# Performance work log

Hardware: AMD Instinct MI355X
Metric: run time of the kernel (lower is better)

Reference implementation:

```python
import jax, jax.numpy as jnp
import numpy as np

H = 32
W = 32
CIN = 64
GR = 4
CC = 6  # channels_count
N = 2


def build_a(h, w):
    # Faithful replication of the torch buffer construction (incl. overlapping
    # writes into channel 0, which accumulate multiple -1 entries per row).
    num = h * w
    a = np.zeros((num, CC, num), np.float32)
    for i in range(num):
        if (i + 1) % w != 0 and i + 1 < num:
            a[i, 0, i] = 1.0
            a[i, 0, i + 1] = -1.0
        if i + w < num:
            a[i, 1, i] = 1.0
            a[i, 1, i + w] = -1.0
        if (i + 2) % w != 0 and (i + 1) % w != 0 and (i + 2 < num):
            a[i, 2, i] = 1.0
            a[i, 2, i + 2] = -1.0
        if i + 2 * w < num:
            a[i, 3, i] = 1.0
            a[i, 3, i + 2 * w] = -1.0
        if i % w != 0 and i + w < num:
            a[i, 0, i] = 1.0
            a[i, 0, i + w - 1] = -1.0
        if (i + 1) % w != 0 and i + w < num:
            a[i, 0, i] = 1.0
            a[i, 0, i + w + 1] = -1.0
    for k in range(CC):
        a[-1, k, -1] = 1.0
    return jnp.asarray(a)


def conv2d(x, w, b, pad):
    y = jax.lax.conv_general_dilated(
        x, w, window_strides=(1, 1), padding=[(pad, pad), (pad, pad)],
        dimension_numbers=('NCHW', 'OIHW', 'NCHW'))
    return y + b[None, :, None, None]


def setup_inputs() -> dict:
    key = jax.random.key(0)
    ks = jax.random.split(key, 20)
    s = 0.05
    d = {
        'x': jax.random.normal(ks[0], (N, CIN, H, W), jnp.float32),
        'a': build_a(H, W),
        # grad branch: conv3x3 CIN->CIN, conv3x3 CIN->CC*GR
        'gw1': jax.random.normal(ks[1], (CIN, CIN, 3, 3), jnp.float32) * s,
        'gb1': jnp.zeros((CIN,), jnp.float32),
        'gw2': jax.random.normal(ks[2], (CC * GR, CIN, 3, 3), jnp.float32) * s,
        'gb2': jnp.zeros((CC * GR,), jnp.float32),
        # att branch (sigmoid at end)
        'aw1': jax.random.normal(ks[3], (CIN, CIN, 3, 3), jnp.float32) * s,
        'ab1': jnp.zeros((CIN,), jnp.float32),
        'aw2': jax.random.normal(ks[4], (CC * GR, CIN, 3, 3), jnp.float32) * s,
        'ab2': jnp.zeros((CC * GR,), jnp.float32),
        # SE branch: 1x1 CIN->CIN//2, 1x1 CIN//2->GR
        'sw1': jax.random.normal(ks[5], (CIN // 2, CIN, 1, 1), jnp.float32) * s,
        'sb1': jnp.zeros((CIN // 2,), jnp.float32),
        'sw2': jax.random.normal(ks[6], (GR, CIN // 2, 1, 1), jnp.float32) * s,
        'sb2': jnp.zeros((GR,), jnp.float32),
        # GroupNorm(1, GR) affine params
        'gn_g': jnp.ones((GR,), jnp.float32),
        'gn_b': jnp.zeros((GR,), jnp.float32),
        # post conv3x3 GR->128
        'pw': jax.random.normal(ks[7], (128, GR, 3, 3), jnp.float32) * s,
        'pb': jnp.zeros((128,), jnp.float32),
    }
    return d


def reference(x, a, gw1, gb1, gw2, gb2, aw1, ab1, aw2, ab2,
              sw1, sb1, sw2, sb2, gn_g, gn_b, pw, pb):
    n, c, h, w = x.shape
    hw = h * w
    lrelu = lambda t: jax.nn.leaky_relu(t, 0.01)

    att = jax.nn.sigmoid(conv2d(lrelu(conv2d(x, aw1, ab1, 1)), aw2, ab2, 1))
    grad = conv2d(lrelu(conv2d(x, gw1, gb1, 1)), gw2, gb2, 1)
    pooled = jnp.mean(x, axis=(2, 3), keepdims=True)
    se = jax.nn.sigmoid(conv2d(lrelu(conv2d(pooled, sw1, sb1, 0)), sw2, sb2, 0))  # [n,GR,1,1]

    b = n * GR
    att = att.reshape(b, CC, hw, 1).transpose(0, 2, 1, 3)   # [b, hw, CC, 1]
    grad = grad.reshape(b, CC, hw, 1).transpose(0, 2, 1, 3)  # [b, hw, CC, 1]

    A = (a[None] * att).reshape(b, hw * CC, hw)   # [b, hw*CC, hw]
    B = (grad * att).reshape(b, hw * CC)          # [b, hw*CC]

    ATA = jnp.einsum('bkm,bkn->bmn', A, A) + 1e-12 * jnp.eye(hw, dtype=x.dtype)
    ATB = jnp.einsum('bkm,bk->bm', A, B)[..., None]
    sol = jnp.linalg.solve(ATA, ATB).reshape(n, GR, h, w)

    # GroupNorm(1, GR): normalize over all (GR,h,w) per sample, per-channel affine
    mu = jnp.mean(sol, axis=(1, 2, 3), keepdims=True)
    var = jnp.var(sol, axis=(1, 2, 3), keepdims=True)
    y = (sol - mu) / jnp.sqrt(var + 1e-5)
    y = y * gn_g[None, :, None, None] + gn_b[None, :, None, None]

    y = se * y
    return conv2d(y, pw, pb, 1)
```

## Files before the change

kernel.cpp:

```cpp
#include <hip/hip_runtime.h>
#include <math.h>

#define HW 1024

__device__ __forceinline__ float lrelu(float v) { return v > 0.f ? v : 0.01f * v; }
__device__ __forceinline__ float sigmoidf(float v) { return 1.f / (1.f + expf(-v)); }

__device__ __forceinline__ float block_reduce(float v, float* red, int tid) {
#pragma unroll
  for (int off = 32; off > 0; off >>= 1) v += __shfl_xor(v, off, 64);
  if ((tid & 63) == 0) red[tid >> 6] = v;
  __syncthreads();
  float s = red[0] + red[1] + red[2] + red[3];
  __syncthreads();
  return s;
}

template <int MODE>
__device__ __forceinline__ void conv_direct(
    const float* __restrict__ X,
    const float* __restrict__ Wb,
    float bias,
    float* __restrict__ outp,
    int rb) {
  __shared__ float4 sred[192];
  int tid = threadIdx.x;
  int w = tid >> 6, l = tid & 63;
  int c4 = l & 7, ry = l >> 3;
  int r = rb * 8 + ry;
  int c0 = c4 * 4;
  int cL = (c4 == 0) ? 0 : c0 - 1;
  int cR = (c4 == 7) ? 31 : c0 + 4;
  float lmf = (c4 == 0) ? 0.f : 1.f;
  float rmf = (c4 == 7) ? 0.f : 1.f;
  int rrc[3];
  float rmk[3];
#pragma unroll
  for (int dr = 0; dr < 3; ++dr) {
    int rr = r - 1 + dr;
    bool ok = (unsigned)rr < 32u;
    rrc[dr] = ok ? rr * 32 : 0;
    rmk[dr] = ok ? 1.f : 0.f;
  }
  const float* Xw = X + w * 16 * HW;
  const float* Wp = Wb + w * 16 * 9;
  float ax = 0.f, ay = 0.f, az = 0.f, aq = 0.f;
#pragma unroll 4
  for (int i = 0; i < 16; ++i) {
    const float* pl = Xw + i * HW;
    const float* wq = Wp + i * 9;
#pragma unroll
    for (int dr = 0; dr < 3; ++dr) {
      const float* rp = pl + rrc[dr];
      float4 m = *(const float4*)(rp + c0);
      float L = rp[cL] * lmf;
      float R = rp[cR] * rmf;
      float w0 = wq[dr * 3 + 0] * rmk[dr];
      float w1 = wq[dr * 3 + 1] * rmk[dr];
      float w2 = wq[dr * 3 + 2] * rmk[dr];
      ax += w0 * L   + w1 * m.x + w2 * m.y;
      ay += w0 * m.x + w1 * m.y + w2 * m.z;
      az += w0 * m.y + w1 * m.z + w2 * m.w;
      aq += w0 * m.z + w1 * m.w + w2 * R;
    }
  }
  if (w > 0) sred[(w - 1) * 64 + l] = make_float4(ax, ay, az, aq);
  __syncthreads();
  if (w == 0) {
    float4 p0 = sred[l], p1 = sred[64 + l], p2 = sred[128 + l];
    float o0 = ax + p0.x + p1.x + p2.x + bias;
    float o1 = ay + p0.y + p1.y + p2.y + bias;
    float o2 = az + p0.z + p1.z + p2.z + bias;
    float o3 = aq + p0.w + p1.w + p2.w + bias;
    if (MODE == 0) { o0 = lrelu(o0); o1 = lrelu(o1); o2 = lrelu(o2); o3 = lrelu(o3); }
    else if (MODE == 1) { o0 = sigmoidf(o0); o1 = sigmoidf(o1); o2 = sigmoidf(o2); o3 = sigmoidf(o3); }
    *(float4*)(outp + r * 32 + c0) = make_float4(o0, o1, o2, o3);
  }
}

__global__ __launch_bounds__(256) void conv64_pool(const float* __restrict__ x,
    const float* __restrict__ aw, const float* __restrict__ ab,
    const float* __restrict__ gw, const float* __restrict__ gb,
    float* __restrict__ t1, float* __restrict__ pooled) {
  int bx = blockIdx.x;
  if (bx < 1024) {
    int co = bx & 63, t = bx >> 6, rb = t & 3, g = t >> 2;
    int br = g >> 1, n = g & 1;
    conv_direct<0>(x + n * 64 * HW,
                   (br ? gw : aw) + co * 576,
                   (br ? gb : ab)[co],
                   t1 + (g * 64 + co) * HW, rb);
  } else {
    __shared__ float red[4];
    int p = bx - 1024;
    const float* px = x + p * HW;
    int tid = threadIdx.x;
    float s = px[tid] + px[tid + 256] + px[tid + 512] + px[tid + 768];
    s = block_reduce(s, red, tid);
    if (tid == 0) pooled[p] = s * (1.f / 1024.f);
  }
}

__global__ __launch_bounds__(256) void conv24_k(const float* __restrict__ t1,
    const float* __restrict__ aw2, const float* __restrict__ ab2,
    const float* __restrict__ gw2, const float* __restrict__ gb2,
    float* __restrict__ attb, float* __restrict__ gradb) {
  int bx = blockIdx.x;
  int co = bx % 24, t = bx / 24, rb = t & 3, g = t >> 2;
  int br = g >> 1, n = g & 1;
  const float* X = t1 + g * 64 * HW;
  const float* Wb = (br ? gw2 : aw2) + co * 576;
  float bias = (br ? gb2 : ab2)[co];
  float* outp = (br ? gradb : attb) + (n * 24 + co) * HW;
  if (br) conv_direct<2>(X, Wb, bias, outp, rb);
  else    conv_direct<1>(X, Wb, bias, outp, rb);
}

__global__ __launch_bounds__(256, 1) void cg_solve(const float* __restrict__ att,
    const float* __restrict__ grad, float* __restrict__ sol,
    int maxit, float tolrel) {
  int b = blockIdx.x, tid = threadIdx.x;
  __shared__ float As[7 * 1088];
  __shared__ __align__(16) float ubuf[1152];
  __shared__ float red[8];
  float* OD1  = As;
  float* OD2  = As + 1 * 1088;
  float* OD30 = As + 2 * 1088;
  float* OD31 = As + 3 * 1088;
  float* OD32 = As + 4 * 1088;
  float* OD33 = As + 5 * 1088;
  float* OD64 = As + 6 * 1088;
  for (int i = tid; i < 448; i += 256) As[(i >> 6) * 1088 + (i & 63)] = 0.f;
  if (tid < 64) { ubuf[tid] = 0.f; ubuf[1088 + tid] = 0.f; }

  const float* attb = att + b * 6 * HW;
  const float* grdb = grad + b * 6 * HW;
  const int m0 = 4 * tid;
  const int idx0 = 64 + m0;
  float rk[4], d0v[4];
#pragma unroll
  for (int k = 0; k < 4; ++k) {
    int m = m0 + k;
    int mr = m & 31;
    bool p1 = (mr != 31) && (m < 1023);
    bool p2 = (mr != 0) && (m < 992);
    bool p3 = (mr != 31) && (m < 992);
    bool dd = p1 | p2 | p3;
    bool c1 = m < 992;
    bool c2 = (mr != 30) && (mr != 31) && (m < 1022);
    bool c3 = m < 960;
    float a0 = attb[m],            g0 = grdb[m];
    float a1 = attb[HW + m],       g1 = grdb[HW + m];
    float a2 = attb[2 * HW + m],   g2 = grdb[2 * HW + m];
    float a3 = attb[3 * HW + m],   g3 = grdb[3 * HW + m];
    float u0 = a0 * a0, t0 = u0 * g0;
    float u1 = a1 * a1, t1 = u1 * g1;
    float u2 = a2 * a2, t2 = u2 * g2;
    float u3 = a3 * a3, t3 = u3 * g3;
    float u0m1 = 0.f, t0m1 = 0.f; bool p1m1 = false, p2m1 = false, p3m1 = false;
    if (m >= 1) {
      int j = m - 1; int jr = j & 31;
      p1m1 = (jr != 31) && (j < 1023); p2m1 = (jr != 0) && (j < 992); p3m1 = (jr != 31) && (j < 992);
      float a = attb[j], g = grdb[j]; u0m1 = a * a; t0m1 = u0m1 * g;
    }
    float u0m31 = 0.f, t0m31 = 0.f; bool p2m31 = false, p3m31 = false;
    if (m >= 31) {
      int j = m - 31; int jr = j & 31;
      p2m31 = (jr != 0) && (j < 992); p3m31 = (jr != 31) && (j < 992);
      float a = attb[j], g = grdb[j]; u0m31 = a * a; t0m31 = u0m31 * g;
    }
    float u0m33 = 0.f, t0m33 = 0.f; bool p3m33 = false;
    if (m >= 33) {
      int j = m - 33; int jr = j & 31;
      p3m33 = (jr != 31) && (j < 992);
      float a = attb[j], g = grdb[j]; u0m33 = a * a; t0m33 = u0m33 * g;
    }
    float u1m32 = 0.f, t1m32 = 0.f; bool c1m32 = false;
    if (m >= 32) {
      int j = m - 32; c1m32 = (j < 992);
      float a = attb[HW + j], g = grdb[HW + j]; u1m32 = a * a; t1m32 = u1m32 * g;
    }
    float u2m2 = 0.f, t2m2 = 0.f; bool c2m2 = false;
    if (m >= 2) {
      int j = m - 2; int jr = j & 31;
      c2m2 = (jr != 30) && (jr != 31) && (j < 1022);
      float a = attb[2 * HW + j], g = grdb[2 * HW + j]; u2m2 = a * a; t2m2 = u2m2 * g;
    }
    float u3m64 = 0.f, t3m64 = 0.f; bool c3m64 = false;
    if (m >= 64) {
      int j = m - 64; c3m64 = (j < 960);
      float a = attb[3 * HW + j], g = grdb[3 * HW + j]; u3m64 = a * a; t3m64 = u3m64 * g;
    }
    float d0 = (dd ? u0 : 0.f) + (c1 ? u1 : 0.f) + (c2 ? u2 : 0.f) + (c3 ? u3 : 0.f)
             + (p1m1 ? u0m1 : 0.f) + (p2m31 ? u0m31 : 0.f) + (p3m33 ? u0m33 : 0.f)
             + (c1m32 ? u1m32 : 0.f) + (c2m2 ? u2m2 : 0.f) + (c3m64 ? u3m64 : 0.f) + 1e-12f;
    float rhs = (dd ? t0 : 0.f) + (c1 ? t1 : 0.f) + (c2 ? t2 : 0.f) + (c3 ? t3 : 0.f)
              - (p1m1 ? t0m1 : 0.f) - (p2m31 ? t0m31 : 0.f) - (p3m33 ? t0m33 : 0.f)
              - (c1m32 ? t1m32 : 0.f) - (c2m2 ? t2m2 : 0.f) - (c3m64 ? t3m64 : 0.f);
    if (m == 1023) {
      float a4 = attb[4 * HW + 1023], g4 = grdb[4 * HW + 1023];
      float a5 = attb[5 * HW + 1023], g5 = grdb[5 * HW + 1023];
      d0 += u0 + u1 + u2 + u3 + a4 * a4 + a5 * a5;
      rhs += t0 + t1 + t2 + t3 + a4 * a4 * g4 + a5 * a5 * g5;
    }
    int idx = idx0 + k;
    OD1[idx]  = p1 ? -u0 : 0.f;
    OD31[idx] = p2 ? -u0 : 0.f;
    OD33[idx] = p3 ? -u0 : 0.f;
    OD2[idx]  = (c2 ? -u2 : 0.f) + ((p2m31 && p3m31) ? u0m31 : 0.f);
    OD30[idx] = (p1m1 && p2m1) ? u0m1 : 0.f;
    OD32[idx] = (c1 ? -u1 : 0.f) + ((p1m1 && p3m1) ? u0m1 : 0.f);
    OD64[idx] = c3 ? -u3 : 0.f;
    d0v[k] = d0;
    rk[k] = rhs;
  }
  __syncthreads();

  float c1p[4], c1m[4], c2p[4], c2m[4], c30p[4], c30m[4], c31p[4], c31m[4];
  float c32p[4], c32m[4], c33p[4], c33m[4], c64p[4], c64m[4];
#pragma unroll
  for (int k = 0; k < 4; ++k) {
    int idx = idx0 + k;
    c1p[k]  = OD1[idx];  c1m[k]  = OD1[idx - 1];
    c2p[k]  = OD2[idx];  c2m[k]  = OD2[idx - 2];
    c30p[k] = OD30[idx]; c30m[k] = OD30[idx - 30];
    c31p[k] = OD31[idx]; c31m[k] = OD31[idx - 31];
    c32p[k] = OD32[idx]; c32m[k] = OD32[idx - 32];
    c33p[k] = OD33[idx]; c33m[k] = OD33[idx - 33];
    c64p[k] = OD64[idx]; c64m[k] = OD64[idx - 64];
  }

  float xk[4] = {0.f, 0.f, 0.f, 0.f};
  float uk[4], wk[4], pk[4], sk[4];
  const float* base = ubuf + idx0;
  int wv = tid >> 6, lane = tid & 63;

#define SPMV_AND_DOTS(GAM, DLT)                                              \
  {                                                                          \
    float2 A01 = *(const float2*)(base - 2);                                 \
    float2 A67 = *(const float2*)(base + 4);                                 \
    float2 B01 = *(const float2*)(base + 30);                                \
    float4 B25 = *(const float4*)(base + 32);                                \
    float  B6  = base[36];                                                   \
    float  C0  = base[-33];                                                  \
    float4 C14 = *(const float4*)(base - 32);                                \
    float2 C56 = *(const float2*)(base - 28);                                \
    float4 Dp  = *(const float4*)(base + 64);                                \
    float4 Ep  = *(const float4*)(base - 64);                                \
    float Aa[8] = {A01.x, A01.y, uk[0], uk[1], uk[2], uk[3], A67.x, A67.y};  \
    float Ba[7] = {B01.x, B01.y, B25.x, B25.y, B25.z, B25.w, B6};            \
    float Ca[7] = {C0, C14.x, C14.y, C14.z, C14.w, C56.x, C56.y};            \
    float Da[4] = {Dp.x, Dp.y, Dp.z, Dp.w};                                  \
    float Ea[4] = {Ep.x, Ep.y, Ep.z, Ep.w};                                  \
    GAM = 0.f; DLT = 0.f;                                                    \
    _Pragma("unroll")                                                        \
    for (int k = 0; k < 4; ++k) {                                            \
      float v = d0v[k] * uk[k];                                              \
      v += c1p[k]  * Aa[3 + k] + c1m[k]  * Aa[1 + k];                        \
      v += c2p[k]  * Aa[4 + k] + c2m[k]  * Aa[k];                            \
      v += c30p[k] * Ba[k]     + c30m[k] * Ca[3 + k];                        \
      v += c31p[k] * Ba[1 + k] + c31m[k] * Ca[2 + k];                        \
      v += c32p[k] * Ba[2 + k] + c32m[k] * Ca[1 + k];                        \
      v += c33p[k] * Ba[3 + k] + c33m[k] * Ca[k];                            \
      v += c64p[k] * Da[k]     + c64m[k] * Ea[k];                            \
      wk[k] = v;                                                             \
      GAM += rk[k] * uk[k];                                                  \
      DLT += v * uk[k];                                                      \
    }                                                                        \
    _Pragma("unroll")                                                        \
    for (int off = 32; off > 0; off >>= 1) {                                 \
      GAM += __shfl_xor(GAM, off, 64);                                       \
      DLT += __shfl_xor(DLT, off, 64);                                       \
    }                                                                        \
    if (lane == 0) { red[wv] = GAM; red[4 + wv] = DLT; }                     \
    __syncthreads();                                                         \
    GAM = red[0] + red[1] + red[2] + red[3];                                 \
    DLT = red[4] + red[5] + red[6] + red[7];                                 \
  }

#pragma unroll
  for (int k = 0; k < 4; ++k) uk[k] = rk[k] / d0v[k];
  *(float4*)(ubuf + idx0) = make_float4(uk[0], uk[1], uk[2], uk[3]);
  __syncthreads();
  float gamma, delta;
  SPMV_AND_DOTS(gamma, delta);
  if (!(fabsf(delta) > 0.f)) { goto done; }
  {
    float alpha = gamma / delta;
    float stop = gamma * tolrel;
#pragma unroll
    for (int k = 0; k < 4; ++k) {
      pk[k] = uk[k]; sk[k] = wk[k];
      xk[k] += alpha * pk[k];
      rk[k] -= alpha * sk[k];
    }
    float gamma_prev = gamma, alpha_prev = alpha;
    for (int it = 1; it < maxit; ++it) {
#pragma unroll
      for (int k = 0; k < 4; ++k) uk[k] = rk[k] / d0v[k];
      *(float4*)(ubuf + idx0) = make_float4(uk[0], uk[1], uk[2], uk[3]);
      __syncthreads();
      float g, dlt;
      SPMV_AND_DOTS(g, dlt);
      float beta = g / gamma_prev;
      float denom = dlt - beta * g / alpha_prev;
      if (!(fabsf(denom) > 0.f)) break;
      float alpha = g / denom;
#pragma unroll
      for (int k = 0; k < 4; ++k) {
        pk[k] = uk[k] + beta * pk[k];
        sk[k] = wk[k] + beta * sk[k];
        xk[k] += alpha * pk[k];
        rk[k] -= alpha * sk[k];
      }
      gamma_prev = g; alpha_prev = alpha;
      if (!(g > stop)) break;
    }
  }
done:
#pragma unroll
  for (int k = 0; k < 4; ++k) sol[b * HW + m0 + k] = xk[k];
#undef SPMV_AND_DOTS
}

__global__ __launch_bounds__(256) void gnorm_postconv(
    const float* __restrict__ sol, const float* __restrict__ pooled,
    const float* __restrict__ sw1, const float* __restrict__ sb1,
    const float* __restrict__ sw2, const float* __restrict__ sb2,
    const float* __restrict__ gn_g, const float* __restrict__ gn_b,
    const float* __restrict__ pw, const float* __restrict__ pb,
    float* __restrict__ out) {
  int bx = blockIdx.x;
  int n = bx >> 7, co = bx & 127;
  int tid = threadIdx.x;
  __shared__ float yp[4 * 1024];
  __shared__ float wb[36];
  __shared__ float red[4];
  __shared__ float s1[32];
  __shared__ float seg[4];
  if (tid < 36) wb[tid] = pw[co * 36 + tid];
  const float* s = sol + n * 4096;
  float v[16];
  float sum = 0.f, ssq = 0.f;
#pragma unroll
  for (int k = 0; k < 16; ++k) {
    v[k] = s[tid + 256 * k];
    sum += v[k];
    ssq += v[k] * v[k];
  }
  sum = block_reduce(sum, red, tid);
  ssq = block_reduce(ssq, red, tid);
  if (tid < 32) {
    float acc = sb1[tid];
    for (int ci = 0; ci < 64; ++ci) acc += sw1[tid * 64 + ci] * pooled[n * 64 + ci];
    s1[tid] = lrelu(acc);
  }
  __syncthreads();
  if (tid < 4) {
    float acc = sb2[tid];
    for (int j = 0; j < 32; ++j) acc += sw2[tid * 32 + j] * s1[j];
    seg[tid] = sigmoidf(acc);
  }
  __syncthreads();
  float mu = sum * (1.f / 4096.f);
  float var = ssq * (1.f / 4096.f) - mu * mu;
  float inv = rsqrtf(var + 1e-5f);
#pragma unroll
  for (int k = 0; k < 16; ++k) {
    int m = tid + 256 * k;
    int g = m >> 10;
    float val = (v[k] - mu) * inv * gn_g[g] + gn_b[g];
    yp[m] = val * seg[g];
  }
  __syncthreads();
  float bias = pb[co];
  float acc[4] = {bias, bias, bias, bias};
#pragma unroll
  for (int k = 0; k < 4; ++k) {
    int m = tid + 256 * k;
    int yy = m >> 5, xx = m & 31;
#pragma unroll
    for (int g = 0; g < 4; ++g) {
      const float* pl = yp + g * 1024;
      const float* wc = wb + g * 9;
#pragma unroll
      for (int dy = -1; dy <= 1; ++dy) {
        int y2 = yy + dy;
        if ((unsigned)y2 < 32u) {
          const float* row = pl + y2 * 32;
#pragma unroll
          for (int dx = -1; dx <= 1; ++dx) {
            int x2 = xx + dx;
            if ((unsigned)x2 < 32u) acc[k] += row[x2] * wc[(dy + 1) * 3 + dx + 1];
          }
        }
      }
    }
  }
#pragma unroll
  for (int k = 0; k < 4; ++k) out[(n * 128 + co) * HW + tid + 256 * k] = acc[k];
}

extern "C" void kernel_launch(void* const* d_in, const int* in_sizes, int n_in,
                              void* d_out, int out_size, void* d_ws, size_t ws_size,
                              hipStream_t stream) {
  const float* x   = (const float*)d_in[0];
  const float* gw1 = (const float*)d_in[2];
  const float* gb1 = (const float*)d_in[3];
  const float* gw2 = (const float*)d_in[4];
  const float* gb2 = (const float*)d_in[5];
  const float* aw1 = (const float*)d_in[6];
  const float* ab1 = (const float*)d_in[7];
  const float* aw2 = (const float*)d_in[8];
  const float* ab2 = (const float*)d_in[9];
  const float* sw1 = (const float*)d_in[10];
  const float* sb1 = (const float*)d_in[11];
  const float* sw2 = (const float*)d_in[12];
  const float* sb2 = (const float*)d_in[13];
  const float* gng = (const float*)d_in[14];
  const float* gnb = (const float*)d_in[15];
  const float* pw  = (const float*)d_in[16];
  const float* pb  = (const float*)d_in[17];
  float* out = (float*)d_out;
  float* ws = (float*)d_ws;

  float* t1     = out;
  float* attb   = ws;
  float* gradb  = ws + 49152;
  float* pooled = ws + 98304;
  float* solv   = ws + 98432;

  conv64_pool<<<1152, 256, 0, stream>>>(x, aw1, ab1, gw1, gb1, t1, pooled);
  conv24_k<<<384, 256, 0, stream>>>(t1, aw2, ab2, gw2, gb2, attb, gradb);
  cg_solve<<<8, 256, 0, stream>>>(attb, gradb, solv, 2000, 1e-5f);
  gnorm_postconv<<<256, 256, 0, stream>>>(solv, pooled, sw1, sb1, sw2, sb2,
                                          gng, gnb, pw, pb, out);
}
```

Baseline: 185.8 us.

## Cap CG iterations, stage conv weights in LDS, use DPP neighbor exchange

Lowers the CG iteration cap from 2000 to 600, which cuts worst-case solver work if convergence needs more iterations. The conv kernel now stages weights in shared memory and gets its left and right halo values from neighbouring lanes through DPP row shifts instead of extra global loads. The CG solver precomputes reciprocal diagonals and multiplies instead of dividing. The groupnorm kernel uses float4 loads with a fused scale and shift. The iteration cap can stop the solve before it meets tolerance, and the added syncs in the conv kernel bring a small cost of their own.

After: 150.9 us (median of 2 runs). -18.8%, faster.

```diff
diff --git a/kernel.cpp b/kernel.cpp
--- a/kernel.cpp
+++ b/kernel.cpp
@@ -5,6 +5,15 @@
 
 __device__ __forceinline__ float lrelu(float v) { return v > 0.f ? v : 0.01f * v; }
 __device__ __forceinline__ float sigmoidf(float v) { return 1.f / (1.f + expf(-v)); }
+
+__device__ __forceinline__ float dpp_prev(float x) {
+  return __int_as_float(__builtin_amdgcn_update_dpp(
+      0, __float_as_int(x), 0x111, 0xF, 0xF, true));
+}
+__device__ __forceinline__ float dpp_next(float x) {
+  return __int_as_float(__builtin_amdgcn_update_dpp(
+      0, __float_as_int(x), 0x101, 0xF, 0xF, true));
+}
 
 __device__ __forceinline__ float block_reduce(float v, float* red, int tid) {
 #pragma unroll
@@ -24,15 +33,15 @@
     float* __restrict__ outp,
     int rb) {
   __shared__ float4 sred[192];
+  __shared__ float wl[576];
   int tid = threadIdx.x;
   int w = tid >> 6, l = tid & 63;
   int c4 = l & 7, ry = l >> 3;
   int r = rb * 8 + ry;
   int c0 = c4 * 4;
-  int cL = (c4 == 0) ? 0 : c0 - 1;
-  int cR = (c4 == 7) ? 31 : c0 + 4;
   float lmf = (c4 == 0) ? 0.f : 1.f;
   float rmf = (c4 == 7) ? 0.f : 1.f;
+  if (tid < 144) ((float4*)wl)[tid] = ((const float4*)Wb)[tid];
   int rrc[3];
   float rmk[3];
 #pragma unroll
@@ -42,8 +51,9 @@
     rrc[dr] = ok ? rr * 32 : 0;
     rmk[dr] = ok ? 1.f : 0.f;
   }
+  __syncthreads();
   const float* Xw = X + w * 16 * HW;
-  const float* Wp = Wb + w * 16 * 9;
+  const float* Wp = wl + w * 144;
   float ax = 0.f, ay = 0.f, az = 0.f, aq = 0.f;
 #pragma unroll 4
   for (int i = 0; i < 16; ++i) {
@@ -53,8 +63,8 @@
     for (int dr = 0; dr < 3; ++dr) {
       const float* rp = pl + rrc[dr];
       float4 m = *(const float4*)(rp + c0);
-      float L = rp[cL] * lmf;
-      float R = rp[cR] * rmf;
+      float L = dpp_prev(m.w) * lmf;
+      float R = dpp_next(m.x) * rmf;
       float w0 = wq[dr * 3 + 0] * rmk[dr];
       float w1 = wq[dr * 3 + 1] * rmk[dr];
       float w2 = wq[dr * 3 + 2] * rmk[dr];
@@ -64,6 +74,7 @@
       aq += w0 * m.z + w1 * m.w + w2 * R;
     }
   }
+  __syncthreads();
   if (w > 0) sred[(w - 1) * 64 + l] = make_float4(ax, ay, az, aq);
   __syncthreads();
   if (w == 0) {
@@ -137,7 +148,7 @@
   const float* grdb = grad + b * 6 * HW;
   const int m0 = 4 * tid;
   const int idx0 = 64 + m0;
-  float rk[4], d0v[4];
+  float rk[4], d0v[4], d0r[4];
 #pragma unroll
   for (int k = 0; k < 4; ++k) {
     int m = m0 + k;
@@ -212,6 +223,7 @@
     OD32[idx] = (c1 ? -u1 : 0.f) + ((p1m1 && p3m1) ? u0m1 : 0.f);
     OD64[idx] = c3 ? -u3 : 0.f;
     d0v[k] = d0;
+    d0r[k] = 1.f / d0;
     rk[k] = rhs;
   }
   __syncthreads();
@@ -279,7 +291,7 @@
   }
 
 #pragma unroll
-  for (int k = 0; k < 4; ++k) uk[k] = rk[k] / d0v[k];
+  for (int k = 0; k < 4; ++k) uk[k] = rk[k] * d0r[k];
   *(float4*)(ubuf + idx0) = make_float4(uk[0], uk[1], uk[2], uk[3]);
   __syncthreads();
   float gamma, delta;
@@ -297,7 +309,7 @@
     float gamma_prev = gamma, alpha_prev = alpha;
     for (int it = 1; it < maxit; ++it) {
 #pragma unroll
-      for (int k = 0; k < 4; ++k) uk[k] = rk[k] / d0v[k];
+      for (int k = 0; k < 4; ++k) uk[k] = rk[k] * d0r[k];
       *(float4*)(ubuf + idx0) = make_float4(uk[0], uk[1], uk[2], uk[3]);
       __syncthreads();
       float g, dlt;
@@ -333,20 +345,21 @@
   int bx = blockIdx.x;
   int n = bx >> 7, co = bx & 127;
   int tid = threadIdx.x;
-  __shared__ float yp[4 * 1024];
+  __shared__ __align__(16) float yp[4 * 1024];
   __shared__ float wb[36];
   __shared__ float red[4];
   __shared__ float s1[32];
   __shared__ float seg[4];
   if (tid < 36) wb[tid] = pw[co * 36 + tid];
-  const float* s = sol + n * 4096;
-  float v[16];
+  const float4* s4 = (const float4*)(sol + n * 4096);
+  float4 v4[4];
   float sum = 0.f, ssq = 0.f;
 #pragma unroll
-  for (int k = 0; k < 16; ++k) {
-    v[k] = s[tid + 256 * k];
-    sum += v[k];
-    ssq += v[k] * v[k];
+  for (int k = 0; k < 4; ++k) {
+    float4 t = s4[tid + 256 * k];
+    v4[k] = t;
+    sum += t.x + t.y + t.z + t.w;
+    ssq += t.x * t.x + t.y * t.y + t.z * t.z + t.w * t.w;
   }
   sum = block_reduce(sum, red, tid);
   ssq = block_reduce(ssq, red, tid);
@@ -366,11 +379,17 @@
   float var = ssq * (1.f / 4096.f) - mu * mu;
   float inv = rsqrtf(var + 1e-5f);
 #pragma unroll
-  for (int k = 0; k < 16; ++k) {
-    int m = tid + 256 * k;
-    int g = m >> 10;
-    float val = (v[k] - mu) * inv * gn_g[g] + gn_b[g];
-    yp[m] = val * seg[g];
+  for (int k = 0; k < 4; ++k) {
+    int q = tid + 256 * k;
+    int g = q >> 8;
+    float sA = inv * gn_g[g] * seg[g];
+    float sB = (gn_b[g] - mu * inv * gn_g[g]) * seg[g];
+    float4 t = v4[k];
+    t.x = t.x * sA + sB;
+    t.y = t.y * sA + sB;
+    t.z = t.z * sA + sB;
+    t.w = t.w * sA + sB;
+    ((float4*)yp)[q] = t;
   }
   __syncthreads();
   float bias = pb[co];
@@ -432,7 +451,7 @@
 
   conv64_pool<<<1152, 256, 0, stream>>>(x, aw1, ab1, gw1, gb1, t1, pooled);
   conv24_k<<<384, 256, 0, stream>>>(t1, aw2, ab2, gw2, gb2, attb, gradb);
-  cg_solve<<<8, 256, 0, stream>>>(attb, gradb, solv, 2000, 1e-5f);
+  cg_solve<<<8, 256, 0, stream>>>(attb, gradb, solv, 600, 1e-5f);
   gnorm_postconv<<<256, 256, 0, stream>>>(solv, pooled, sw1, sb1, sw2, sb2,
                                           gng, gnb, pw, pb, out);
 }
```
